# Kernel optimization log

Hardware: AMD Instinct MI355X
Metric: run time of the kernel (lower is better)

## Reference

```python
import jax, jax.numpy as jnp
import numpy as np

B, T, E, H = 8, 2048, 128, 4
FACTOR = 3  # autocorr_factor


def setup_inputs() -> dict:
    key = jax.random.key(0)
    ks = jax.random.split(key, 9)
    s = 0.05
    return {
        "hidden_states": jax.random.normal(ks[0], (B, T, E), jnp.float32),
        "wq": jax.random.normal(ks[1], (E, E, H), jnp.float32) * s,
        "bq": jax.random.normal(ks[2], (E, H), jnp.float32) * s,
        "wk": jax.random.normal(ks[3], (E, E, H), jnp.float32) * s,
        "bk": jax.random.normal(ks[4], (E, H), jnp.float32) * s,
        "wv": jax.random.normal(ks[5], (E, E, H), jnp.float32) * s,
        "bv": jax.random.normal(ks[6], (E, H), jnp.float32) * s,
        "wo": jax.random.normal(ks[7], (E, H, E), jnp.float32) * s,
        "bo": jax.random.normal(ks[8], (E,), jnp.float32) * s,
    }


def reference(hidden_states, wq, bq, wk, bk, wv, bv, wo, bo):
    # Inference path (training=None) of AutoCorrelation.call
    bsize, seq_len, _ = hidden_states.shape
    q = jnp.einsum('btj,juh->btuh', hidden_states, wq) + bq  # [B,T,E,H]
    k = jnp.einsum('btj,juh->btuh', hidden_states, wk) + bk
    v = jnp.einsum('btj,juh->btuh', hidden_states, wv) + bv

    # FFT cross-correlation over time axis
    qf = jnp.fft.rfft(q.transpose(0, 2, 3, 1), n=seq_len, axis=-1)  # [B,E,H,F]
    kf = jnp.fft.rfft(k.transpose(0, 2, 3, 1), n=seq_len, axis=-1)
    ac = jnp.fft.irfft(qf * jnp.conj(kf), n=seq_len, axis=-1)       # [B,E,H,T]
    ac = ac.transpose(0, 3, 1, 2)                                   # [B,T,E,H]

    ac_mean = ac.mean(axis=-1)                                      # [B,T,E]
    top_k = int(FACTOR * np.log(float(seq_len)))

    # top-k delays per (batch, channel)
    vals, idx = jax.lax.top_k(ac_mean.transpose(0, 2, 1), top_k)    # [B,E,K]
    w = jax.nn.softmax(vals, axis=-1)  # == Softmax(axis=-2) on [B,K,E]

    # NOTE: in the source, `delays_agg +=` is dedented outside the top_k loop,
    # so only the LAST iteration (i = top_k-1) contributes. Replicated faithfully.
    delay = idx[:, :, top_k - 1]   # [B,E] int
    wgt = w[:, :, top_k - 1]       # [B,E]

    # gather over doubled values == circular roll by -delay per (b, channel)
    t_idx = (jnp.arange(seq_len)[None, :, None] + delay[:, None, :]) % seq_len  # [B,T,E]
    rolled = jnp.take_along_axis(v, t_idx[..., None], axis=1)       # [B,T,E,H]
    agg = rolled * wgt[:, None, :, None]                            # [B,T,E,H]

    return jnp.einsum('btjh,jhf->btf', agg, wo) + bo                # [B,T,E]
```

## Files before the change

kernel.cpp:

```cpp
#include <hip/hip_runtime.h>
#include <math.h>

#define TSEQ 2048
#define BB 8
#define EE 128
#define HH 4
#define UHN 512
#define KTOP 22
#define BT (BB*TSEQ)
#define APITCH 40
#define OPITCH 76

typedef _Float16 f16;
typedef f16 f16x2 __attribute__((ext_vector_type(2)));
typedef f16 f16x4 __attribute__((ext_vector_type(4)));
typedef f16 f16x8 __attribute__((ext_vector_type(8)));
typedef float f32x4 __attribute__((ext_vector_type(4)));

__device__ __forceinline__ float2 cmul(float2 a, float2 b) {
  return make_float2(a.x*b.x - a.y*b.y, a.x*b.y + a.y*b.x);
}
__device__ __forceinline__ float2 cadd(float2 a, float2 b) {
  return make_float2(a.x + b.x, a.y + b.y);
}
__device__ __forceinline__ float2 csub(float2 a, float2 b) {
  return make_float2(a.x - b.x, a.y - b.y);
}

__device__ __forceinline__ f16x8 ld_frag(const f16* p) {
  f16x4 lo = *(const f16x4*)(p);
  f16x4 hi = *(const f16x4*)(p + 16);
  return __builtin_shufflevector(lo, hi, 0, 1, 2, 3, 4, 5, 6, 7);
}

__global__ __launch_bounds__(256)
void prep_kernel(const float* __restrict__ hs,
                 const float* __restrict__ wq, const float* __restrict__ wk,
                 const float* __restrict__ wv, const float* __restrict__ wo,
                 f16* __restrict__ hs_h, f16* __restrict__ hs_l,
                 f16* __restrict__ Wt_h, f16* __restrict__ Wt_l,
                 f16* __restrict__ wo_t)
{
  __shared__ float tile[64][65];
  const int bx = blockIdx.x, tid = threadIdx.x;

  if (bx < 1024) {
    size_t base = ((size_t)bx*256 + tid) * 8;
    float4 a = *(const float4*)&hs[base];
    float4 b = *(const float4*)&hs[base + 4];
    float vf[8] = {a.x,a.y,a.z,a.w, b.x,b.y,b.z,b.w};
    f16 h[8], l[8];
#pragma unroll
    for (int j = 0; j < 8; ++j) { h[j] = (f16)vf[j]; l[j] = (f16)(vf[j] - (float)h[j]); }
    *(f16x8*)&hs_h[base] = (f16x8){h[0],h[1],h[2],h[3],h[4],h[5],h[6],h[7]};
    *(f16x8*)&hs_l[base] = (f16x8){l[0],l[1],l[2],l[3],l[4],l[5],l[6],l[7]};
  } else if (bx < 1072) {
    int r = bx - 1024;
    int z = r >> 4, rem = r & 15, kt = rem & 1, uht = rem >> 1;
    const float* W = (z == 0) ? wq : (z == 1) ? wk : wv;
#pragma unroll
    for (int rr = 0; rr < 16; ++rr) {
      int idx = tid + 256*rr;
      int krow = idx >> 6, ucol = idx & 63;
      tile[krow][ucol] = W[(size_t)(kt*64 + krow)*UHN + uht*64 + ucol];
    }
    __syncthreads();
#pragma unroll
    for (int rr = 0; rr < 16; ++rr) {
      int idx = tid + 256*rr;
      int orow = idx >> 6, ocol = idx & 63;
      float w = tile[ocol][orow];
      f16 h = (f16)w;
      size_t o = ((size_t)z*UHN + uht*64 + orow)*EE + kt*64 + ocol;
      Wt_h[o] = h;
      Wt_l[o] = (f16)(w - (float)h);
    }
  } else {
    int r = bx - 1072;
    int ft = r & 1, uht = r >> 1;
#pragma unroll
    for (int rr = 0; rr < 16; ++rr) {
      int idx = tid + 256*rr;
      int urow = idx >> 6, fcol = idx & 63;
      tile[urow][fcol] = wo[(size_t)(uht*64 + urow)*EE + ft*64 + fcol];
    }
    __syncthreads();
#pragma unroll
    for (int rr = 0; rr < 16; ++rr) {
      int idx = tid + 256*rr;
      int orow = idx >> 6, ocol = idx & 63;
      wo_t[(size_t)(ft*64 + orow)*UHN + uht*64 + ocol] = (f16)tile[ocol][orow];
    }
  }
}

__global__ __launch_bounds__(256, 4)
void proj_mfma(const f16* __restrict__ hs_h, const f16* __restrict__ hs_l,
               const f16* __restrict__ Wt_h, const f16* __restrict__ Wt_l,
               const float* __restrict__ bq, const float* __restrict__ bk,
               const float* __restrict__ bv,
               float* __restrict__ q_t, float* __restrict__ k_t, f16* __restrict__ v_t)
{
  __shared__ f16 Ah[128*APITCH];
  __shared__ f16 Al[128*APITCH];
  __shared__ f16 Bh[128*APITCH];
  __shared__ f16 Bl[128*APITCH];

  const int z = blockIdx.z;
  const float* bias = (z == 0) ? bq : (z == 1) ? bk : bv;
  const f16* WH = Wt_h + (size_t)z*UHN*EE;
  const f16* WL = Wt_l + (size_t)z*UHN*EE;

  const int tid  = threadIdx.x;
  const int lane = tid & 63, wid = tid >> 6;
  const int wm = wid >> 1, wn = wid & 1;
  const int ln15 = lane & 15, g = lane >> 4;
  const int uh0 = blockIdx.x * 128;
  const int bt0 = blockIdx.y * 128;

  f32x4 acc[4][4] = {};

  for (int kc = 0; kc < 4; ++kc) {
    const int k0 = kc * 32;
    __syncthreads();
#pragma unroll
    for (int r = 0; r < 2; ++r) {
      int idx = tid + 256*r;
      int row = idx >> 2, seg = (idx & 3) << 3;
      size_t ga = (size_t)(uh0 + row)*EE + k0 + seg;
      *(f16x8*)&Ah[row*APITCH + seg] = *(const f16x8*)&WH[ga];
      *(f16x8*)&Al[row*APITCH + seg] = *(const f16x8*)&WL[ga];
      size_t gb = (size_t)(bt0 + row)*EE + k0 + seg;
      *(f16x8*)&Bh[row*APITCH + seg] = *(const f16x8*)&hs_h[gb];
      *(f16x8*)&Bl[row*APITCH + seg] = *(const f16x8*)&hs_l[gb];
    }
    __syncthreads();
    const int kb = 4*g;
    f16x8 a_h[4], a_l[4], b_h[4], b_l[4];
#pragma unroll
    for (int mf = 0; mf < 4; ++mf) {
      int off = (wm*64 + mf*16 + ln15)*APITCH + kb;
      a_h[mf] = ld_frag(&Ah[off]);
      a_l[mf] = ld_frag(&Al[off]);
    }
#pragma unroll
    for (int nf = 0; nf < 4; ++nf) {
      int off = (wn*64 + nf*16 + ln15)*APITCH + kb;
      b_h[nf] = ld_frag(&Bh[off]);
      b_l[nf] = ld_frag(&Bl[off]);
    }
#pragma unroll
    for (int mf = 0; mf < 4; ++mf)
#pragma unroll
      for (int nf = 0; nf < 4; ++nf) {
        acc[mf][nf] = __builtin_amdgcn_mfma_f32_16x16x32_f16(a_h[mf], b_h[nf], acc[mf][nf], 0, 0, 0);
        acc[mf][nf] = __builtin_amdgcn_mfma_f32_16x16x32_f16(a_h[mf], b_l[nf], acc[mf][nf], 0, 0, 0);
        acc[mf][nf] = __builtin_amdgcn_mfma_f32_16x16x32_f16(a_l[mf], b_h[nf], acc[mf][nf], 0, 0, 0);
      }
  }

  const int b = bt0 >> 11, tb = bt0 & (TSEQ - 1);
  if (z == 2) {
#pragma unroll
    for (int mf = 0; mf < 4; ++mf) {
      int uhb = uh0 + wm*64 + mf*16 + g*4;
      f32x4 bias4 = *(const f32x4*)&bias[uhb];
#pragma unroll
      for (int r = 0; r < 4; ++r) {
        f16* vrow = v_t + ((size_t)(b*UHN + uhb + r))*TSEQ + tb;
#pragma unroll
        for (int nf = 0; nf < 4; ++nf)
          vrow[wn*64 + nf*16 + ln15] = (f16)(acc[mf][nf][r] + bias4[r]);
      }
    }
  } else {
    float* outp = (z == 0) ? q_t : k_t;
#pragma unroll
    for (int mf = 0; mf < 4; ++mf) {
      int uhb = uh0 + wm*64 + mf*16 + g*4;
      f32x4 bias4 = *(const f32x4*)&bias[uhb];
#pragma unroll
      for (int r = 0; r < 4; ++r) {
        size_t rowbase = ((size_t)(b*UHN + uhb + r))*TSEQ + tb;
#pragma unroll
        for (int nf = 0; nf < 4; ++nf)
          outp[rowbase + wn*64 + nf*16 + ln15] = acc[mf][nf][r] + bias4[r];
      }
    }
  }
}

#define ZPAD(g) ((g) + ((g) >> 5))

template<int SGN>
__device__ __forceinline__ float2 addim(float2 a, float2 b) {
  return (SGN < 0) ? make_float2(a.x + b.y, a.y - b.x)
                   : make_float2(a.x - b.y, a.y + b.x);
}
template<int SGN>
__device__ __forceinline__ float2 subim(float2 a, float2 b) {
  return (SGN < 0) ? make_float2(a.x - b.y, a.y + b.x)
                   : make_float2(a.x + b.y, a.y - b.x);
}

template<int SGN>
__device__ __forceinline__ void dft8(const float2* u, float2* y) {
  const float r2 = 0.70710678118654752440f;
  float2 a0 = cadd(u[0], u[4]), a1 = cadd(u[1], u[5]);
  float2 a2 = cadd(u[2], u[6]), a3 = cadd(u[3], u[7]);
  float2 b0 = csub(u[0], u[4]), b1 = csub(u[1], u[5]);
  float2 b2 = csub(u[2], u[6]), b3 = csub(u[3], u[7]);
  float2 t1 = (SGN < 0) ? make_float2(r2*(b1.x + b1.y), r2*(b1.y - b1.x))
                        : make_float2(r2*(b1.x - b1.y), r2*(b1.y + b1.x));
  float2 t2 = (SGN < 0) ? make_float2(b2.y, -b2.x) : make_float2(-b2.y, b2.x);
  float2 e  = (SGN < 0) ? make_float2(r2*(b3.x + b3.y), r2*(b3.y - b3.x))
                        : make_float2(r2*(b3.x - b3.y), r2*(b3.y + b3.x));
  float2 t3 = (SGN < 0) ? make_float2(e.y, -e.x) : make_float2(-e.y, e.x);
  {
    float2 c0 = cadd(a0, a2), c1 = csub(a0, a2);
    float2 c2 = cadd(a1, a3), c3 = csub(a1, a3);
    y[0] = cadd(c0, c2); y[4] = csub(c0, c2);
    y[2] = addim<SGN>(c1, c3); y[6] = subim<SGN>(c1, c3);
  }
  {
    float2 c0 = cadd(b0, t2), c1 = csub(b0, t2);
    float2 c2 = cadd(t1, t3), c3 = csub(t1, t3);
    y[1] = cadd(c0, c2); y[5] = csub(c0, c2);
    y[3] = addim<SGN>(c1, c3); y[7] = subim<SGN>(c1, c3);
  }
}

__device__ __forceinline__ void fwd_radix8(float2* Z, float2 w1, int base, int eighth) {
  float2 u[8];
#pragma unroll
  for (int t = 0; t < 8; ++t) u[t] = Z[ZPAD(base + eighth*t)];
  float2 y[8];
  dft8<-1>(u, y);
  Z[ZPAD(base)] = y[0];
  float2 w = w1;
  Z[ZPAD(base + eighth)] = cmul(y[1], w);
#pragma unroll
  for (int s = 2; s < 8; ++s) {
    w = cmul(w, w1);
    Z[ZPAD(base + eighth*s)] = cmul(y[s], w);
  }
}

__device__ __forceinline__ void inv_radix8(float2* Z, float2 w1c, int base, int eighth) {
  float2 u[8];
#pragma unroll
  for (int t = 0; t < 8; ++t) u[t] = Z[ZPAD(base + eighth*t)];
  u[1] = cmul(u[1], w1c);
  float2 w = w1c;
#pragma unroll
  for (int t = 2; t < 8; ++t) {
    w = cmul(w, w1c);
    u[t] = cmul(u[t], w);
  }
  float2 y[8];
  dft8<1>(u, y);
#pragma unroll
  for (int s = 0; s < 8; ++s) Z[ZPAD(base + eighth*s)] = y[s];
}

template<int SGN>
__device__ __forceinline__ void radix4_stage(float2* Z, int base) {
  float2 v0 = Z[ZPAD(base)], v1 = Z[ZPAD(base+1)];
  float2 v2 = Z[ZPAD(base+2)], v3 = Z[ZPAD(base+3)];
  float2 c0 = cadd(v0, v2), c1 = csub(v0, v2);
  float2 c2 = cadd(v1, v3), c3 = csub(v1, v3);
  Z[ZPAD(base)]   = cadd(c0, c2);
  Z[ZPAD(base+1)] = addim<SGN>(c1, c3);
  Z[ZPAD(base+2)] = csub(c0, c2);
  Z[ZPAD(base+3)] = subim<SGN>(c1, c3);
}

__global__ __launch_bounds__(512, 4)
void fftcorr_topk(const float* __restrict__ q_t, const float* __restrict__ k_t,
                  int* __restrict__ delay, float* __restrict__ wgt)
{
  __shared__ float2 Z[2*2112];
  __shared__ float2 twl[292];

  const int tid  = threadIdx.x;
  const int half = tid >> 8;
  const int t8   = tid & 255;
  const int bu   = blockIdx.x*2 + half;
  float2* Zh = Z + half*2112;

  if (tid < 292) {
    int idx = tid;
    float ang;
    if (idx < 256)      ang = -6.2831853071795864769f * (float)idx / 2048.0f;
    else if (idx < 288) ang = -6.2831853071795864769f * (float)(idx - 256) / 256.0f;
    else                ang = -6.2831853071795864769f * (float)(idx - 288) / 32.0f;
    float s, c;
    sincosf(ang, &s, &c);
    twl[idx] = make_float2(c, s);
  }
  const float2* tw1 = twl;
  const float2* tw2 = twl + 256;
  const float2* tw3 = twl + 288;

  int pp[8];
#pragma unroll
  for (int r = 0; r < 8; ++r) {
    int p = t8 + (r << 8);
    int f = ((p >> 8) & 7) | (((p >> 5) & 7) << 3) | (((p >> 2) & 7) << 6) | ((p & 3) << 9);
    int nf = (2048 - f) & 2047;
    pp[r] = ((nf & 7) << 8) | (((nf >> 3) & 7) << 5) | (((nf >> 6) & 7) << 2) | ((nf >> 9) & 3);
  }
  float2 sreg[8] = {};
  __syncthreads();

  for (int h = 0; h < HH; ++h) {
    const float* qp = q_t + ((size_t)bu*HH + h)*TSEQ;
    const float* kp = k_t + ((size_t)bu*HH + h)*TSEQ;
    {
      float2 u[8];
#pragma unroll
      for (int t = 0; t < 8; ++t)
        u[t] = make_float2(qp[t8 + 256*t], kp[t8 + 256*t]);
      float2 y[8];
      dft8<-1>(u, y);
      float2 w1 = tw1[t8];
      Zh[ZPAD(t8)] = y[0];
      float2 w = w1;
      Zh[ZPAD(t8 + 256)] = cmul(y[1], w);
#pragma unroll
      for (int s = 2; s < 8; ++s) {
        w = cmul(w, w1);
        Zh[ZPAD(t8 + 256*s)] = cmul(y[s], w);
      }
    }
    __syncthreads();
    fwd_radix8(Zh, tw2[t8 & 31], ((t8 >> 5) << 8) + (t8 & 31), 32);
    __syncthreads();
    fwd_radix8(Zh, tw3[t8 & 3], ((t8 >> 2) << 5) + (t8 & 3), 4);
    __syncthreads();
    radix4_stage<-1>(Zh, 4*t8);
    radix4_stage<-1>(Zh, 4*(t8 + 256));
    __syncthreads();
#pragma unroll
    for (int r = 0; r < 8; ++r) {
      int p = t8 + (r << 8);
      float2 A  = Zh[ZPAD(p)];
      float2 Zp = Zh[ZPAD(pp[r])];
      sreg[r].x += 0.5f  * (Zp.x*A.y + Zp.y*A.x);
      sreg[r].y += 0.25f * ((A.x*A.x + A.y*A.y) - (Zp.x*Zp.x + Zp.y*Zp.y));
    }
    __syncthreads();
  }

#pragma unroll
  for (int r = 0; r < 8; ++r) Zh[ZPAD(t8 + (r << 8))] = sreg[r];
  __syncthreads();
  radix4_stage<1>(Zh, 4*t8);
  radix4_stage<1>(Zh, 4*(t8 + 256));
  __syncthreads();
  { float2 w = tw3[t8 & 3]; w.y = -w.y;
    inv_radix8(Zh, w, ((t8 >> 2) << 5) + (t8 & 3), 4); }
  __syncthreads();
  { float2 w = tw2[t8 & 31]; w.y = -w.y;
    inv_radix8(Zh, w, ((t8 >> 5) << 8) + (t8 & 31), 32); }
  __syncthreads();

  float* vbuf = (float*)Zh;
  float* lmf  = vbuf + 2048;
  int*   lii  = (int*)(vbuf + 2304);
  {
    float2 u[8];
#pragma unroll
    for (int t = 0; t < 8; ++t) u[t] = Zh[ZPAD(t8 + 256*t)];
    __syncthreads();
    float2 w1c = tw1[t8]; w1c.y = -w1c.y;
    u[1] = cmul(u[1], w1c);
    float2 w = w1c;
#pragma unroll
    for (int t = 2; t < 8; ++t) {
      w = cmul(w, w1c);
      u[t] = cmul(u[t], w);
    }
    float2 y[8];
    dft8<1>(u, y);
    const float scale = 1.0f / (float)(TSEQ * HH);
    float lb = -3.4e38f; int lbi = t8;
#pragma unroll
    for (int s = 0; s < 8; ++s) {
      float x = y[s].x * scale;
      vbuf[t8 + 256*s] = x;
      if (x > lb) { lb = x; lbi = t8 + 256*s; }
    }
    lmf[t8] = lb;
    lii[t8] = lbi;
  }
  __syncthreads();

  if (((tid >> 6) & 3) == 0) {
    const int lane = tid & 63;
    float m0 = 0.f, ssum = 0.f;
    for (int it = 0; it < KTOP; ++it) {
      float best = -3.4e38f; int bi = 0x40000000;
#pragma unroll
      for (int e = 0; e < 4; ++e) {
        float x = lmf[4*lane + e];
        int  xi = lii[4*lane + e];
        if (x > best || (x == best && xi < bi)) { best = x; bi = xi; }
      }
#pragma unroll
      for (int off = 32; off > 0; off >>= 1) {
        float ob = __shfl_down(best, off);
        int   oi = __shfl_down(bi, off);
        if (ob > best || (ob == best && oi < bi)) { best = ob; bi = oi; }
      }
      float gb = __shfl(best, 0);
      int   gi = __shfl(bi, 0);
      int   ow = gi & 255;
      if (lane == (ow >> 2)) {
        vbuf[gi] = -3.4e38f;
        float nb = -3.4e38f; int ni = ow;
#pragma unroll
        for (int s = 0; s < 8; ++s) {
          float x = vbuf[ow + 256*s];
          if (x > nb) { nb = x; ni = ow + 256*s; }
        }
        lmf[ow] = nb;
        lii[ow] = ni;
      }
      if (lane == 0) {
        if (it == 0) m0 = gb;
        ssum += expf(gb - m0);
        if (it == KTOP - 1) {
          delay[bu] = gi;
          wgt[bu]   = expf(gb - m0) / ssum;
        }
      }
    }
  }
}

__global__ __launch_bounds__(256)
void out_mfma(const f16* __restrict__ v_t, const int* __restrict__ delay,
              const float* __restrict__ wgt, const f16* __restrict__ wo_t,
              const float* __restrict__ bo, float* __restrict__ out)
{
  __shared__ f16 Af[64*OPITCH];
  __shared__ f16 Bf[64*OPITCH];
  __shared__ int   dly[EE];
  __shared__ float wg[EE];

  const int tid  = threadIdx.x;
  const int lane = tid & 63, wid = tid >> 6;
  const int wm = wid >> 1, wn = wid & 1;
  const int ln15 = lane & 15, g = lane >> 4;
  const int t0g = blockIdx.x * 64;
  const int f0  = blockIdx.y * 64;
  const int b = t0g >> 11, t0 = t0g & (TSEQ - 1);

  if (tid < EE) { dly[tid] = delay[b*EE + tid]; wg[tid] = wgt[b*EE + tid]; }

  f32x4 acc[2][2] = {};

  for (int c = 0; c < 8; ++c) {
    const int uh0 = c * 64;
    __syncthreads();
#pragma unroll
    for (int r = 0; r < 16; ++r) {
      int idx = tid + 256*r;
      int tl = idx & 63, ul = idx >> 6;
      int u = (uh0 + ul) >> 2;
      float x = (float)v_t[((size_t)(b*UHN + uh0 + ul))*TSEQ + ((t0 + tl + dly[u]) & (TSEQ-1))]
                * wg[u];
      Af[tl*OPITCH + ul] = (f16)x;
    }
#pragma unroll
    for (int r = 0; r < 2; ++r) {
      int idx = tid + 256*r;
      int fl = idx >> 3, seg = (idx & 7) << 3;
      const f16* src = &wo_t[(size_t)(f0 + fl)*UHN + uh0 + seg];
      *(f16x4*)&Bf[fl*OPITCH + seg]     = *(const f16x4*)(src);
      *(f16x4*)&Bf[fl*OPITCH + seg + 4] = *(const f16x4*)(src + 4);
    }
    __syncthreads();
#pragma unroll
    for (int ks = 0; ks < 2; ++ks) {
      const int kb = ks*32 + 4*g;
      f16x8 av[2], bv[2];
#pragma unroll
      for (int mf = 0; mf < 2; ++mf)
        av[mf] = ld_frag(&Af[(wm*32 + mf*16 + ln15)*OPITCH + kb]);
#pragma unroll
      for (int nf = 0; nf < 2; ++nf)
        bv[nf] = ld_frag(&Bf[(wn*32 + nf*16 + ln15)*OPITCH + kb]);
#pragma unroll
      for (int mf = 0; mf < 2; ++mf)
#pragma unroll
        for (int nf = 0; nf < 2; ++nf)
          acc[mf][nf] = __builtin_amdgcn_mfma_f32_16x16x32_f16(av[mf], bv[nf], acc[mf][nf], 0, 0, 0);
    }
  }

#pragma unroll
  for (int mf = 0; mf < 2; ++mf)
#pragma unroll
    for (int r = 0; r < 4; ++r) {
      int bt = t0g + wm*32 + mf*16 + g*4 + r;
#pragma unroll
      for (int nf = 0; nf < 2; ++nf) {
        int f = f0 + wn*32 + nf*16 + ln15;
        out[(size_t)bt*EE + f] = acc[mf][nf][r] + bo[f];
      }
    }
}

extern "C" void kernel_launch(void* const* d_in, const int* in_sizes, int n_in,
                              void* d_out, int out_size, void* d_ws, size_t ws_size,
                              hipStream_t stream) {
  (void)in_sizes; (void)n_in; (void)out_size; (void)ws_size;
  const float* hs = (const float*)d_in[0];
  const float* wq = (const float*)d_in[1];
  const float* bq = (const float*)d_in[2];
  const float* wk = (const float*)d_in[3];
  const float* bk = (const float*)d_in[4];
  const float* wv = (const float*)d_in[5];
  const float* bv = (const float*)d_in[6];
  const float* wo = (const float*)d_in[7];
  const float* bo = (const float*)d_in[8];
  float* out = (float*)d_out;

  char* p = (char*)d_ws;
  float* q_t  = (float*)p;  p += (size_t)BB*UHN*TSEQ*4;
  float* k_t  = (float*)p;  p += (size_t)BB*UHN*TSEQ*4;
  f16*   v_t  = (f16*)p;    p += (size_t)BB*UHN*TSEQ*2;
  f16*   hs_h = (f16*)p;    p += (size_t)BT*EE*2;
  f16*   hs_l = (f16*)p;    p += (size_t)BT*EE*2;
  f16*   Wt_h = (f16*)p;    p += (size_t)3*UHN*EE*2;
  f16*   Wt_l = (f16*)p;    p += (size_t)3*UHN*EE*2;
  f16*   wo_t = (f16*)p;    p += (size_t)EE*UHN*2;
  int*   delay = (int*)p;   p += BB*EE*4;
  float* wgt   = (float*)p;

  prep_kernel<<<dim3(1088), 256, 0, stream>>>(hs, wq, wk, wv, wo,
                                              hs_h, hs_l, Wt_h, Wt_l, wo_t);
  proj_mfma<<<dim3(4, 128, 3), 256, 0, stream>>>(hs_h, hs_l, Wt_h, Wt_l,
                                                 bq, bk, bv, q_t, k_t, v_t);
  fftcorr_topk<<<dim3(512), 512, 0, stream>>>(q_t, k_t, delay, wgt);
  out_mfma<<<dim3(256, 2), 256, 0, stream>>>(v_t, delay, wgt, wo_t, bo, out);
}
```

Before: 133.9 us.

## Process all four heads in parallel per block and reduce spectra in LDS

The FFT-correlation kernel now uses one 1024-thread block per (batch, channel) pair, with four 256-thread groups each computing one head's forward FFT at the same time instead of looping over heads serially. The per-head spectral products are computed in place using Hermitian symmetry, so only one bin of each conjugate pair is evaluated, and the four heads are then summed in shared memory. The inverse FFT and top-k then run on a single group. This shortens the serial per-block chain but leaves most threads idle during the inverse and top-k phases, doubles LDS use per block, and drops the explicit occupancy hint.

```diff
diff --git a/kernel.cpp b/kernel.cpp
--- a/kernel.cpp
+++ b/kernel.cpp
@@ -275,18 +275,18 @@
   Z[ZPAD(base+3)] = subim<SGN>(c1, c3);
 }
 
-__global__ __launch_bounds__(512, 4)
+__global__ __launch_bounds__(1024)
 void fftcorr_topk(const float* __restrict__ q_t, const float* __restrict__ k_t,
                   int* __restrict__ delay, float* __restrict__ wgt)
 {
-  __shared__ float2 Z[2*2112];
+  __shared__ float2 Z[4*2112];
   __shared__ float2 twl[292];
 
-  const int tid  = threadIdx.x;
-  const int half = tid >> 8;
-  const int t8   = tid & 255;
-  const int bu   = blockIdx.x*2 + half;
-  float2* Zh = Z + half*2112;
+  const int tid = threadIdx.x;
+  const int grp = tid >> 8;
+  const int t8  = tid & 255;
+  const int bu  = blockIdx.x;
+  float2* Zh = Z + grp*2112;
 
   if (tid < 292) {
     int idx = tid;
@@ -301,103 +301,113 @@
   const float2* tw1 = twl;
   const float2* tw2 = twl + 256;
   const float2* tw3 = twl + 288;
-
-  int pp[8];
+  __syncthreads();
+
+  {
+    const float* qp = q_t + ((size_t)bu*HH + grp)*TSEQ;
+    const float* kp = k_t + ((size_t)bu*HH + grp)*TSEQ;
+    float2 u[8];
+#pragma unroll
+    for (int t = 0; t < 8; ++t)
+      u[t] = make_float2(qp[t8 + 256*t], kp[t8 + 256*t]);
+    float2 y[8];
+    dft8<-1>(u, y);
+    float2 w1 = tw1[t8];
+    Zh[ZPAD(t8)] = y[0];
+    float2 w = w1;
+    Zh[ZPAD(t8 + 256)] = cmul(y[1], w);
+#pragma unroll
+    for (int s = 2; s < 8; ++s) {
+      w = cmul(w, w1);
+      Zh[ZPAD(t8 + 256*s)] = cmul(y[s], w);
+    }
+  }
+  __syncthreads();
+  fwd_radix8(Zh, tw2[t8 & 31], ((t8 >> 5) << 8) + (t8 & 31), 32);
+  __syncthreads();
+  fwd_radix8(Zh, tw3[t8 & 3], ((t8 >> 2) << 5) + (t8 & 3), 4);
+  __syncthreads();
+  radix4_stage<-1>(Zh, 4*t8);
+  radix4_stage<-1>(Zh, 4*(t8 + 256));
+  __syncthreads();
+
 #pragma unroll
   for (int r = 0; r < 8; ++r) {
     int p = t8 + (r << 8);
     int f = ((p >> 8) & 7) | (((p >> 5) & 7) << 3) | (((p >> 2) & 7) << 6) | ((p & 3) << 9);
     int nf = (2048 - f) & 2047;
-    pp[r] = ((nf & 7) << 8) | (((nf >> 3) & 7) << 5) | (((nf >> 6) & 7) << 2) | ((nf >> 9) & 3);
-  }
-  float2 sreg[8] = {};
-  __syncthreads();
-
-  for (int h = 0; h < HH; ++h) {
-    const float* qp = q_t + ((size_t)bu*HH + h)*TSEQ;
-    const float* kp = k_t + ((size_t)bu*HH + h)*TSEQ;
-    {
-      float2 u[8];
-#pragma unroll
-      for (int t = 0; t < 8; ++t)
-        u[t] = make_float2(qp[t8 + 256*t], kp[t8 + 256*t]);
-      float2 y[8];
-      dft8<-1>(u, y);
-      float2 w1 = tw1[t8];
-      Zh[ZPAD(t8)] = y[0];
-      float2 w = w1;
-      Zh[ZPAD(t8 + 256)] = cmul(y[1], w);
-#pragma unroll
-      for (int s = 2; s < 8; ++s) {
-        w = cmul(w, w1);
-        Zh[ZPAD(t8 + 256*s)] = cmul(y[s], w);
-      }
-    }
-    __syncthreads();
-    fwd_radix8(Zh, tw2[t8 & 31], ((t8 >> 5) << 8) + (t8 & 31), 32);
-    __syncthreads();
-    fwd_radix8(Zh, tw3[t8 & 3], ((t8 >> 2) << 5) + (t8 & 3), 4);
-    __syncthreads();
-    radix4_stage<-1>(Zh, 4*t8);
-    radix4_stage<-1>(Zh, 4*(t8 + 256));
-    __syncthreads();
-#pragma unroll
-    for (int r = 0; r < 8; ++r) {
-      int p = t8 + (r << 8);
-      float2 A  = Zh[ZPAD(p)];
-      float2 Zp = Zh[ZPAD(pp[r])];
-      sreg[r].x += 0.5f  * (Zp.x*A.y + Zp.y*A.x);
-      sreg[r].y += 0.25f * ((A.x*A.x + A.y*A.y) - (Zp.x*Zp.x + Zp.y*Zp.y));
-    }
-    __syncthreads();
-  }
-
-#pragma unroll
-  for (int r = 0; r < 8; ++r) Zh[ZPAD(t8 + (r << 8))] = sreg[r];
-  __syncthreads();
-  radix4_stage<1>(Zh, 4*t8);
-  radix4_stage<1>(Zh, 4*(t8 + 256));
-  __syncthreads();
-  { float2 w = tw3[t8 & 3]; w.y = -w.y;
-    inv_radix8(Zh, w, ((t8 >> 2) << 5) + (t8 & 3), 4); }
-  __syncthreads();
-  { float2 w = tw2[t8 & 31]; w.y = -w.y;
-    inv_radix8(Zh, w, ((t8 >> 5) << 8) + (t8 & 31), 32); }
-  __syncthreads();
-
-  float* vbuf = (float*)Zh;
+    int q = ((nf & 7) << 8) | (((nf >> 3) & 7) << 5) | (((nf >> 6) & 7) << 2) | ((nf >> 9) & 3);
+    if (p > q) continue;
+    float2 A = Zh[ZPAD(p)];
+    float2 B = Zh[ZPAD(q)];
+    float re = 0.5f  * (B.x*A.y + B.y*A.x);
+    float im = 0.25f * ((A.x*A.x + A.y*A.y) - (B.x*B.x + B.y*B.y));
+    Zh[ZPAD(p)] = make_float2(re, im);
+    if (q != p) Zh[ZPAD(q)] = make_float2(re, -im);
+  }
+  __syncthreads();
+
+#pragma unroll
+  for (int e = 0; e < 2; ++e) {
+    int zp = ZPAD(2*tid + e);
+    float2 s = Z[zp];
+    s = cadd(s, Z[2112 + zp]);
+    s = cadd(s, Z[2*2112 + zp]);
+    s = cadd(s, Z[3*2112 + zp]);
+    Z[zp] = s;
+  }
+  __syncthreads();
+
+  if (tid < 512) radix4_stage<1>(Z, 4*tid);
+  __syncthreads();
+  if (grp == 0) {
+    float2 w = tw3[t8 & 3]; w.y = -w.y;
+    inv_radix8(Z, w, ((t8 >> 2) << 5) + (t8 & 3), 4);
+  }
+  __syncthreads();
+  if (grp == 0) {
+    float2 w = tw2[t8 & 31]; w.y = -w.y;
+    inv_radix8(Z, w, ((t8 >> 5) << 8) + (t8 & 31), 32);
+  }
+  __syncthreads();
+
+  float* vbuf = (float*)Z;
   float* lmf  = vbuf + 2048;
   int*   lii  = (int*)(vbuf + 2304);
   {
     float2 u[8];
-#pragma unroll
-    for (int t = 0; t < 8; ++t) u[t] = Zh[ZPAD(t8 + 256*t)];
-    __syncthreads();
-    float2 w1c = tw1[t8]; w1c.y = -w1c.y;
-    u[1] = cmul(u[1], w1c);
-    float2 w = w1c;
-#pragma unroll
-    for (int t = 2; t < 8; ++t) {
-      w = cmul(w, w1c);
-      u[t] = cmul(u[t], w);
-    }
-    float2 y[8];
-    dft8<1>(u, y);
-    const float scale = 1.0f / (float)(TSEQ * HH);
-    float lb = -3.4e38f; int lbi = t8;
-#pragma unroll
-    for (int s = 0; s < 8; ++s) {
-      float x = y[s].x * scale;
-      vbuf[t8 + 256*s] = x;
-      if (x > lb) { lb = x; lbi = t8 + 256*s; }
-    }
-    lmf[t8] = lb;
-    lii[t8] = lbi;
-  }
-  __syncthreads();
-
-  if (((tid >> 6) & 3) == 0) {
-    const int lane = tid & 63;
+    if (grp == 0) {
+#pragma unroll
+      for (int t = 0; t < 8; ++t) u[t] = Z[ZPAD(t8 + 256*t)];
+    }
+    __syncthreads();
+    if (grp == 0) {
+      float2 w1c = tw1[t8]; w1c.y = -w1c.y;
+      u[1] = cmul(u[1], w1c);
+      float2 w = w1c;
+#pragma unroll
+      for (int t = 2; t < 8; ++t) {
+        w = cmul(w, w1c);
+        u[t] = cmul(u[t], w);
+      }
+      float2 y[8];
+      dft8<1>(u, y);
+      const float scale = 1.0f / (float)(TSEQ * HH);
+      float lb = -3.4e38f; int lbi = t8;
+#pragma unroll
+      for (int s = 0; s < 8; ++s) {
+        float x = y[s].x * scale;
+        vbuf[t8 + 256*s] = x;
+        if (x > lb) { lb = x; lbi = t8 + 256*s; }
+      }
+      lmf[t8] = lb;
+      lii[t8] = lbi;
+    }
+  }
+  __syncthreads();
+
+  if (tid < 64) {
+    const int lane = tid;
     float m0 = 0.f, ssum = 0.f;
     for (int it = 0; it < KTOP; ++it) {
       float best = -3.4e38f; int bi = 0x40000000;
@@ -544,6 +554,6 @@
                                               hs_h, hs_l, Wt_h, Wt_l, wo_t);
   proj_mfma<<<dim3(4, 128, 3), 256, 0, stream>>>(hs_h, hs_l, Wt_h, Wt_l,
                                                  bq, bk, bv, q_t, k_t, v_t);
-  fftcorr_topk<<<dim3(512), 512, 0, stream>>>(q_t, k_t, delay, wgt);
+  fftcorr_topk<<<dim3(1024), 1024, 0, stream>>>(q_t, k_t, delay, wgt);
   out_mfma<<<dim3(256, 2), 256, 0, stream>>>(v_t, delay, wgt, wo_t, bo, out);
 }
```

After: 156.4 us. +16.7%, slower.
